# Performance work log

Measured on AMD Instinct MI355X. Metric: run time of the kernel, lower is better.

## Reference

```python
import jax, jax.numpy as jnp
import numpy as np

B, T, H = 2, 2048, 1024
NH_R, HD_R = 4, 256            # RWKV6 heads / head_dim
EXP, HD_M = 2, 64
DI = EXP * H                   # mamba inner = 2048
NH_M = DI // HD_M              # 32 mamba heads
DS = 128                       # mamba d_state
CK = 4                         # causal conv kernel
FFN = 4 * H
EPS = 1e-6


def rms(x, w, eps=EPS):
    return w * x * jax.lax.rsqrt(jnp.mean(x * x, -1, keepdims=True) + eps)


def setup_inputs() -> dict:
    key = jax.random.key(0)
    ks = iter(jax.random.split(key, 32))
    def w(shape, scale=0.02):
        return jax.random.normal(next(ks), shape, jnp.float32) * scale
    return dict(
        x=w((B, T, H), 1.0),
        ln_w=jnp.ones((H,), jnp.float32),
        r_w=w((H, H)), k_w=w((H, H)), v_w=w((H, H)), g_w=w((H, H)), dw_w=w((H, H)),
        u=w((NH_R, HD_R), 0.5),
        gn_w=jnp.ones((H,), jnp.float32),
        o_w=w((H, H)),
        in_proj=w((H, 2 * DI + 2 * DS + NH_M)),
        conv_w=w((DI + 2 * DS, CK), 0.1),
        conv_b=jnp.zeros((DI + 2 * DS,), jnp.float32),
        dt_bias=w((NH_M,), 0.1),
        A_log=jnp.log(jnp.arange(1, NH_M + 1, dtype=jnp.float32)),
        D_m=w((NH_M,), 0.5),
        m_norm_w=jnp.ones((DI,), jnp.float32),
        out_proj=w((DI, H)),
        gate_w=jnp.zeros((2 * H, 1), jnp.float32),   # zero-init per module
        gate_b=jnp.zeros((1,), jnp.float32),         # logit(0.5) = 0
        ffn_ln_w=jnp.ones((H,), jnp.float32),
        ffn_w1=w((H, FFN)),
        ffn_w2=w((FFN, H)),
    )


def _rwkv6(nx, r_w, k_w, v_w, g_w, dw_w, u, gn_w, o_w):
    r = (nx @ r_w).reshape(B, T, NH_R, HD_R)
    k = (nx @ k_w).reshape(B, T, NH_R, HD_R)
    v = (nx @ v_w).reshape(B, T, NH_R, HD_R)
    g = jax.nn.silu(nx @ g_w)                                  # output gate
    wdec = jnp.exp(-jnp.exp(nx @ dw_w)).reshape(B, T, NH_R, HD_R)  # data-dep decay in (0,1)
    tm = lambda a: a.transpose(1, 0, 2, 3)                     # [T,B,h,d]

    def step(S, inp):  # S: [B,h,K,V]
        rt, kt, vt, wt = inp
        kv = kt[..., :, None] * vt[..., None, :]
        o = jnp.einsum('bhk,bhkv->bhv', rt, S + u[..., :, None] * kv)
        return wt[..., :, None] * S + kv, o

    S0 = jnp.zeros((B, NH_R, HD_R, HD_R), nx.dtype)
    _, o = jax.lax.scan(step, S0, (tm(r), tm(k), tm(v), tm(wdec)))
    o = o.transpose(1, 0, 2, 3)                                # [B,T,h,d]
    o = o * jax.lax.rsqrt(jnp.mean(o * o, -1, keepdims=True) + EPS)  # per-head RMS (group norm)
    o = o.reshape(B, T, H) * gn_w
    return (o * g) @ o_w


def _mamba2(nx, in_proj, conv_w, conv_b, dt_bias, A_log, D_m, m_norm_w, out_proj):
    zxbcdt = nx @ in_proj
    z, xBC, dt = jnp.split(zxbcdt, [DI, 2 * DI + 2 * DS], axis=-1)
    xp = jnp.pad(xBC, ((0, 0), (CK - 1, 0), (0, 0)))           # causal depthwise conv
    xBC = sum(xp[:, i:i + T, :] * conv_w[:, i] for i in range(CK)) + conv_b
    xBC = jax.nn.silu(xBC)
    xm, Bm, Cm = jnp.split(xBC, [DI, DI + DS], axis=-1)
    xm = xm.reshape(B, T, NH_M, HD_M)
    dt = jax.nn.softplus(dt + dt_bias)                          # [B,T,nh]
    A = -jnp.exp(A_log)                                         # [nh]

    def step(h, inp):  # h: [B,nh,hd,ds]
        xt, Bt, Ct, dtt = inp
        h = h * jnp.exp(dtt * A)[..., None, None] + (dtt[..., None] * xt)[..., None] * Bt[:, None, None, :]
        y = jnp.einsum('bhds,bs->bhd', h, Ct)
        return h, y

    h0 = jnp.zeros((B, NH_M, HD_M, DS), nx.dtype)
    _, y = jax.lax.scan(step, h0, (xm.transpose(1, 0, 2, 3), Bm.transpose(1, 0, 2), Cm.transpose(1, 0, 2), dt.transpose(1, 0, 2)))
    y = y.transpose(1, 0, 2, 3) + D_m[None, None, :, None] * xm
    y = y.reshape(B, T, DI)
    y = rms(y * jax.nn.silu(z), m_norm_w)                       # gated RMSNorm
    return y @ out_proj


def reference(x, ln_w, r_w, k_w, v_w, g_w, dw_w, u, gn_w, o_w,
              in_proj, conv_w, conv_b, dt_bias, A_log, D_m, m_norm_w, out_proj,
              gate_w, gate_b, ffn_ln_w, ffn_w1, ffn_w2):
    nx = rms(x, ln_w)
    o_r = _rwkv6(nx, r_w, k_w, v_w, g_w, dw_w, u, gn_w, o_w)
    o_m = _mamba2(nx, in_proj, conv_w, conv_b, dt_bias, A_log, D_m, m_norm_w, out_proj)
    gate = jax.nn.sigmoid(jnp.concatenate([o_r, o_m], -1) @ gate_w + gate_b)  # [B,T,1]
    x = x + gate * o_r + (1.0 - gate) * o_m
    x = x + jax.nn.gelu(rms(x, ffn_ln_w) @ ffn_w1, approximate=False) @ ffn_w2
    return x
```

## Files before the change

### kernel.cpp

```cpp
#include <hip/hip_runtime.h>
#include <hip/hip_bf16.h>
#include <stdint.h>

#define B_ 2
#define T_ 2048
#define H_ 1024
#define M_ 4096
#define DI 2048
#define DS 128
#define CONVD 2304
#define LD2 4480
#define EPS_ 1e-6f

typedef __bf16 bf16x8 __attribute__((ext_vector_type(8)));
typedef float f32x4 __attribute__((ext_vector_type(4)));
typedef uint32_t u32x4 __attribute__((ext_vector_type(4)));

__device__ __forceinline__ unsigned short f2bfu(float f) {
    union { float f; uint32_t u; } a; a.f = f;
    uint32_t r = a.u + 0x7FFFu + ((a.u >> 16) & 1u);
    return (unsigned short)(r >> 16);
}
__device__ __forceinline__ float bfu2f(unsigned short u) {
    union { uint32_t u; float f; } a; a.u = ((uint32_t)u) << 16; return a.f;
// ... 288 lines not shown
                bg[n] = *(const bf16x8*)((const char*)Bs + (lin ^ ((col & 7) << 4)));
            }
#pragma unroll
            for (int m = 0; m < 4; m++)
#pragma unroll
                for (int n = 0; n < 4; n++)
                    acc[m][n] = __builtin_amdgcn_mfma_f32_16x16x32_bf16(af[m], bg[n], acc[m][n], 0, 0, 0);
        }
    }
    const int seg = n0 >> 10;
#pragma unroll
    for (int m = 0; m < 4; m++) {
#pragma unroll
        for (int r = 0; r < 4; r++) {
            size_t row = (size_t)(m0 + wm + m * 16 + fg * 4 + r);
#pragma unroll
            for (int n = 0; n < 4; n++) {
                int gcol = n0 + wn + n * 16 + fr;
                float v = acc[m][n][r];
                if (n0 < 5120) {
                    size_t idx = row * 1024 + (gcol & 1023);
                    if (seg == 0) RB[idx] = f2bfu(v);
                    else if (seg == 1) KB[idx] = f2bfu(v);
                    else if (seg == 2) VB[idx] = f2bfu(v);
                    else if (seg == 3) GB[idx] = f2bfu(siluf(v));
                    else WF[idx] = expf(-expf(v));
                } else {
                    C2B[row * 4480 + (gcol - 5120)] = f2bfu(v);
                }
            }
        }
    }
}

__global__ __launch_bounds__(256) void k_rwkv_prep(unsigned short* __restrict__ RB, unsigned short* __restrict__ KB,
                                                   const float* __restrict__ WF, const float* __restrict__ u,
                                                   unsigned short* __restrict__ KDt, unsigned short* __restrict__ QLb,
                                                   float* __restrict__ DDb) {
    __shared__ float red[16][257];
    __shared__ float red2[16][17];
    const int c = blockIdx.x, bh = blockIdx.y;
    const int b = bh >> 2, h = bh & 3;
    const int k = threadIdx.x;
    const size_t m0 = (size_t)b * T_ + c * 16;
    const int hk = h * 256 + k;
    const float uv = u[hk];
    float Q = 1.f;
    float kd[16];
#pragma unroll
    for (int s = 0; s < 16; s++) {
        size_t off = (m0 + s) * H_ + hk;
        float r = bfu2f(RB[off]);
        float kv = bfu2f(KB[off]);
        float w = WF[off];
        RB[off] = f2bfu(r * Q);
        Q = fmaxf(Q * w, 1e-35f);
        float kdv = kv / Q;
        kd[s] = kdv;
        KB[off] = f2bfu(kdv);
        red[s][k] = r * uv * kv;
    }
    QLb[((size_t)(b * 128 + c)) * 1024 + hk] = f2bfu(Q);
    size_t kt0 = (((size_t)(b * 128 + c)) * 1024 + hk) * 16;
#pragma unroll
    for (int s = 0; s < 16; s++) KDt[kt0 + s] = f2bfu(kd[s]);
    __syncthreads();
    {
        int s = threadIdx.x >> 4, part = threadIdx.x & 15;
        float ps = 0.f;
#pragma unroll
        for (int j = 0; j < 16; j++) ps += red[s][part * 16 + j];
        red2[s][part] = ps;
    }
    __syncthreads();
    if (threadIdx.x < 32) {
        int s = threadIdx.x & 15, half = threadIdx.x >> 4;
        float d = 0.f;
#pragma unroll
        for (int j = 0; j < 8; j++) d += red2[s][half * 8 + j];
        DDb[(((size_t)bh * 128 + c) * 2 + half) * 16 + s] = d;
    }
}

__global__ __launch_bounds__(256) void k_rwkv_carry(const unsigned short* __restrict__ KD, const unsigned short* __restrict__ VB,
                                                    const unsigned short* __restrict__ QLb, unsigned short* __restrict__ Scc) {
    __shared__ unsigned short kds[16][256];
    __shared__ float lv[16][4];
    const int vg = blockIdx.x, bh = blockIdx.y;
    const int b = bh >> 2, h = bh & 3;
    const int k = threadIdx.x;
    const int hk = h * 256 + k;
    const size_t baseM = (size_t)b * T_;
    float s0 = 0.f, s1 = 0.f, s2 = 0.f, s3 = 0.f;
    for (int c = 0; c < 128; ++c) {
        size_t m0 = baseM + c * 16;
        if ((c & 7) == 0 && c > 0) {
            int cc = c >> 3;
            size_t sb = ((size_t)(bh * 16 + cc) * 256 + vg * 4) * 256 + k;
            Scc[sb] = f2bfu(s0); Scc[sb + 256] = f2bfu(s1);
            Scc[sb + 512] = f2bfu(s2); Scc[sb + 768] = f2bfu(s3);
        }
        __syncthreads();
#pragma unroll
        for (int it = 0; it < 2; ++it) {
            int i = threadIdx.x + it * 256;
            int row = i >> 5, col8 = (i & 31) * 8;
            *(u32x4*)&kds[row][col8] = *(const u32x4*)(KD + (m0 + row) * H_ + h * 256 + col8);
        }
        if (threadIdx.x < 64) {
            int t = threadIdx.x >> 2, j = threadIdx.x & 3;
            lv[t][j] = bfu2f(VB[(m0 + t) * H_ + h * 256 + vg * 4 + j]);
        }
        __syncthreads();
        float a0 = 0.f, a1 = 0.f, a2 = 0.f, a3 = 0.f;
#pragma unroll
        for (int t = 0; t < 16; t++) {
            float kdv = bfu2f(kds[t][k]);
            a0 = fmaf(kdv, lv[t][0], a0);
            a1 = fmaf(kdv, lv[t][1], a1);
            a2 = fmaf(kdv, lv[t][2], a2);
            a3 = fmaf(kdv, lv[t][3], a3);
        }
        float ql = bfu2f(QLb[((size_t)(b * 128 + c)) * 1024 + hk]);
        s0 = (s0 + a0) * ql; s1 = (s1 + a1) * ql;
        s2 = (s2 + a2) * ql; s3 = (s3 + a3) * ql;
    }
}

__global__ __launch_bounds__(256) void k_rwkv_out(const unsigned short* __restrict__ RT, const unsigned short* __restrict__ KD,
                                                  const unsigned short* __restrict__ KDt, const unsigned short* __restrict__ VB,
                                                  const unsigned short* __restrict__ QLb, const float* __restrict__ DDb,
                                                  const unsigned short* __restrict__ Scc,
                                                  float* __restrict__ P0, float* __restrict__ P1) {
    __shared__ unsigned short Sb[64][136];
    __shared__ unsigned short VT[64][24];
    __shared__ unsigned short Ab[16][24];
    __shared__ float dls[16];
    const int tid = threadIdx.x;
    const int vt = blockIdx.x, cc = blockIdx.y;
    const int bh = blockIdx.z >> 1, kh = blockIdx.z & 1;
    const int b = bh >> 2, h = bh & 3;
    const int wave = tid >> 6, lane = tid & 63;
    const int l16 = lane & 15, lq = lane >> 4;
    const int wv0 = wave * 16;
    const int hk0 = h * 256 + kh * 128;
    const int hv = h * 256 + vt * 64;
    const int aoff = (lq < 2) ? lq * 8 : 0;
    float* __restrict__ OP = kh ? P1 : P0;
    f32x4 sreg[8];
    if (cc == 0) {
#pragma unroll
        for (int kt = 0; kt < 8; kt++) sreg[kt] = (f32x4)(0.f);
        for (int i = tid; i < 64 * 136 / 8; i += 256) ((u32x4*)Sb)[i] = (u32x4)(0u);
    } else {
        size_t sbase = ((size_t)(bh * 16 + cc) * 256 + vt * 64);
        for (int i = tid; i < 1024; i += 256) {
            int v = i >> 4, k8 = (i & 15) * 8;
            *(u32x4*)&Sb[v][k8] = *(const u32x4*)(Scc + (sbase + v) * 256 + kh * 128 + k8);
        }
#pragma unroll
        for (int kt = 0; kt < 8; kt++) {
            ushort4 w4 = *(const ushort4*)(Scc + (sbase + wv0 + l16) * 256 + kh * 128 + kt * 16 + lq * 4);
            sreg[kt][0] = bfu2f(w4.x); sreg[kt][1] = bfu2f(w4.y);
            sreg[kt][2] = bfu2f(w4.z); sreg[kt][3] = bfu2f(w4.w);
        }
    }
    __syncthreads();

    for (int fc = 0; fc < 8; ++fc) {
        const int c = cc * 8 + fc;
        const size_t m0 = (size_t)b * T_ + c * 16;
        const size_t bc = (size_t)(b * 128 + c);
        if (fc > 0) __syncthreads();
        {
            int st = tid >> 4, v4 = (tid & 15) * 4;
            ushort4 v4v = *(const ushort4*)(VB + (m0 + st) * H_ + hv + v4);
            VT[v4 + 0][st] = v4v.x; VT[v4 + 1][st] = v4v.y;
            VT[v4 + 2][st] = v4v.z; VT[v4 + 3][st] = v4v.w;
            if (tid < 16) dls[tid] = DDb[(((size_t)bh * 128 + c) * 2 + kh) * 16 + tid];
        }
        __syncthreads();
        const size_t rowA = (m0 + l16) * H_ + hk0;
        bf16x8 rtf[4];
#pragma unroll
        for (int ks = 0; ks < 4; ks++) rtf[ks] = *(const bf16x8*)(RT + rowA + ks * 32 + lq * 8);
        f32x4 Aacc = (f32x4)(0.f);
#pragma unroll
        for (int ks = 0; ks < 4; ks++) {
            bf16x8 kdf = *(const bf16x8*)(KD + rowA + ks * 32 + lq * 8);
            Aacc = __builtin_amdgcn_mfma_f32_16x16x32_bf16(rtf[ks], kdf, Aacc, 0, 0, 0);
        }
        f32x4 oacc = (f32x4)(0.f);
#pragma unroll
        for (int ks = 0; ks < 4; ks++) {
            bf16x8 sbf = *(const bf16x8*)(&Sb[wv0 + l16][ks * 32 + lq * 8]);
            oacc = __builtin_amdgcn_mfma_f32_16x16x32_bf16(rtf[ks], sbf, oacc, 0, 0, 0);
        }
#pragma unroll
        for (int r = 0; r < 4; r++) {
            int t = lq * 4 + r, s = l16;
            float av = (s < t) ? Aacc[r] : ((s == t) ? dls[t] : 0.f);
            Ab[t][s] = f2bfu(av);
        }
        bf16x8 abf_t = *(const bf16x8*)(&Ab[l16][aoff]);
        bf16x8 vtf_t = *(const bf16x8*)(&VT[wv0 + l16][aoff]);
        bf16x8 abf = (lq < 2) ? abf_t : zero8();
        bf16x8 vtf = (lq < 2) ? vtf_t : zero8();
        oacc = __builtin_amdgcn_mfma_f32_16x16x32_bf16(abf, vtf, oacc, 0, 0, 0);
#pragma unroll
        for (int r = 0; r < 4; r++)
            OP[(m0 + lq * 4 + r) * H_ + hv + wv0 + l16] = oacc[r];
#pragma unroll
        for (int kt = 0; kt < 8; kt++) {
            const unsigned short* kp = KDt + (((bc * 1024) + hk0 + kt * 16 + l16) << 4) + aoff;
            bf16x8 kdtf_t = *(const bf16x8*)kp;
            bf16x8 kdtf = (lq < 2) ? kdtf_t : zero8();
            sreg[kt] = __builtin_amdgcn_mfma_f32_16x16x32_bf16(kdtf, vtf, sreg[kt], 0, 0, 0);
            ushort4 q4 = *(const ushort4*)(QLb + bc * 1024 + hk0 + kt * 16 + lq * 4);
            sreg[kt][0] *= bfu2f(q4.x); sreg[kt][1] *= bfu2f(q4.y);
            sreg[kt][2] *= bfu2f(q4.z); sreg[kt][3] *= bfu2f(q4.w);
            ushort4 pk;
            pk.x = f2bfu(sreg[kt][0]); pk.y = f2bfu(sreg[kt][1]);
            pk.z = f2bfu(sreg[kt][2]); pk.w = f2bfu(sreg[kt][3]);
            *(ushort4*)(&Sb[wv0 + l16][kt * 16 + lq * 4]) = pk;
        }
    }
}

__global__ __launch_bounds__(256) void k_rwkv_post(const float* __restrict__ P0, const float* __restrict__ P1,
                                                   const float* __restrict__ gn_w, unsigned short* __restrict__ g_io) {
    int m = blockIdx.x, tid = threadIdx.x;
    int wave = tid >> 6, lane = tid & 63;
    size_t base = (size_t)m * H_ + wave * 256 + lane * 4;
    int col = wave * 256 + lane * 4;
    float4 a = *(const float4*)(P0 + base);
    float4 b4 = *(const float4*)(P1 + base);
    float4 v; v.x = a.x + b4.x; v.y = a.y + b4.y; v.z = a.z + b4.z; v.w = a.w + b4.w;
    float ss = v.x * v.x + v.y * v.y + v.z * v.z + v.w * v.w;
#pragma unroll
    for (int off = 32; off; off >>= 1) ss += __shfl_xor(ss, off);
    float scale = rsqrtf(ss * (1.f / 256.f) + EPS_);
    float4 gn = *(const float4*)(gn_w + col);
    ushort4 gb4 = *(const ushort4*)(g_io + base);
    ushort4 out;
    out.x = f2bfu(v.x * scale * gn.x * bfu2f(gb4.x));
    out.y = f2bfu(v.y * scale * gn.y * bfu2f(gb4.y));
    out.z = f2bfu(v.z * scale * gn.z * bfu2f(gb4.z));
    out.w = f2bfu(v.w * scale * gn.w * bfu2f(gb4.w));
    *(ushort4*)(g_io + base) = out;
}

__global__ __launch_bounds__(256) void k_conv(const unsigned short* __restrict__ C2B, const float* __restrict__ conv_w,
                                              const float* __restrict__ conv_b, unsigned short* __restrict__ XB,
                                              float* __restrict__ BCF) {
    int m = blockIdx.y;
    int c = blockIdx.x * 256 + threadIdx.x;
    int b = m >> 11, t = m & 2047;
    float acc = conv_b[c];
#pragma unroll
    for (int i = 0; i < 4; i++) {
        int tt = t - 3 + i;
        if (tt >= 0) acc = fmaf(bfu2f(C2B[((size_t)(b * T_ + tt)) * LD2 + DI + c]), conv_w[c * 4 + i], acc);
    }
    float r = siluf(acc);
    if (c < DI) XB[(size_t)m * DI + c] = f2bfu(r);
    else BCF[(size_t)m * 256 + (c - DI)] = r;
}

__global__ __launch_bounds__(256) void k_mprep(const unsigned short* __restrict__ C2B,
                                               const float* __restrict__ dt_bias, const float* __restrict__ A_log,
                                               float* __restrict__ DT, float* __restrict__ CD,
                                               float* __restrict__ WS, float* __restrict__ WSC,
                                               float* __restrict__ QJ, float* __restrict__ QLf,
                                               float* __restrict__ QC) {
    __shared__ float sums[128], offs[128], ce[16];
    const int bh = blockIdx.x;
    const int b = bh >> 5, h = bh & 31;
    const int c = threadIdx.x;
    const float A = -expf(A_log[h]);
    const float dtb = dt_bias[h];
    float dloc[16], cdl[16];
    if (c < 128) {
        float acc = 0.f;
#pragma unroll
        for (int s = 0; s < 16; s++) {
            size_t m = (size_t)b * T_ + c * 16 + s;
            float draw = bfu2f(C2B[m * LD2 + 4352 + h]) + dtb;
            float dt = draw > 20.f ? draw : log1pf(expf(draw));
            acc += dt;
            dloc[s] = dt; cdl[s] = acc;
        }
        sums[c] = acc;
    }
    __syncthreads();
    if (threadIdx.x == 0) {
        float run = 0.f;
        for (int i = 0; i < 128; i++) { offs[i] = run; run += sums[i]; }
    }
    __syncthreads();
    if (threadIdx.x < 16) {
        int last = threadIdx.x * 8 + 7;
        ce[threadIdx.x] = offs[last] + sums[last];
    }
    __syncthreads();
    if (c < 128) {
        float off = offs[c];
        float cd15 = off + cdl[15];
        float ceC = ce[c >> 3];
        QLf[bh * 128 + c] = expf(fminf(A * cdl[15], 0.f));
        size_t base = (size_t)bh * 2048 + c * 16;
#pragma unroll
        for (int s = 0; s < 16; s++) {
            float cdg = off + cdl[s];
            DT[base + s] = dloc[s];
            CD[base + s] = cdg;
            QJ[base + s] = expf(fminf(A * (cdg - off), 0.f));
            WS[base + s] = expf(fminf(A * (cd15 - cdg), 0.f)) * dloc[s];
            WSC[base + s] = expf(fminf(A * (ceC - cdg), 0.f)) * dloc[s];
        }
    }
    if (threadIdx.x < 16) {
        float prev = threadIdx.x ? ce[threadIdx.x - 1] : 0.f;
        QC[bh * 16 + threadIdx.x] = expf(fminf(A * (ce[threadIdx.x] - prev), 0.f));
    }
}

__global__ __launch_bounds__(64) void k_amask(const float* __restrict__ BCF,
                                              const float* __restrict__ CD, const float* __restrict__ DT,
                                              const float* __restrict__ A_log,
                                              unsigned short* __restrict__ AM) {
    const int c = blockIdx.x, bh = blockIdx.y;
    const int b = bh >> 5, h = bh & 31;
    const int lane = threadIdx.x;
    const int l16 = lane & 15, lq = lane >> 4;
    const float A = -expf(A_log[h]);
    const size_t m = (size_t)b * T_ + c * 16 + l16;
    f32x4 Aacc = (f32x4)(0.f);
#pragma unroll
    for (int ks = 0; ks < 4; ks++) {
        bf16x8 cf, bf;
        const float* cr = BCF + m * 256 + 128 + ks * 32 + lq * 8;
        const float* br = BCF + m * 256 + ks * 32 + lq * 8;
#pragma unroll
        for (int i = 0; i < 8; i++) { cf[i] = (__bf16)cr[i]; bf[i] = (__bf16)br[i]; }
        Aacc = __builtin_amdgcn_mfma_f32_16x16x32_bf16(cf, bf, Aacc, 0, 0, 0);
    }
    size_t base = ((size_t)bh * 128 + c) * 256;
    size_t tb = (size_t)bh * 2048 + c * 16;
    float cds = CD[tb + l16];
    float dts = DT[tb + l16];
#pragma unroll
    for (int r = 0; r < 4; r++) {
        int j = lq * 4 + r;
        float av = 0.f;
        if (l16 <= j) {
            float cdj = CD[tb + j];
            av = Aacc[r] * expf(fminf(A * (cdj - cds), 0.f)) * dts;
        }
        AM[base + j * 16 + l16] = f2bfu(av);
    }
}

__global__ __launch_bounds__(256) void k_mcarry(const float* __restrict__ BCF, const unsigned short* __restrict__ XB,
                                                const float* __restrict__ WSC, const float* __restrict__ QC,
                                                unsigned short* __restrict__ MSCC) {
    __shared__ float Bsf[64][128];
    __shared__ unsigned short BWt[128][72];
    __shared__ unsigned short XT[16][72];
    __shared__ float wsl[64];
    const int tid = threadIdx.x;
    const int dq = blockIdx.x, bh = blockIdx.y;
    const int b = bh >> 5, h = bh & 31;
    const int wave = tid >> 6, lane = tid & 63;
    const int l16 = lane & 15, lq = lane >> 4;
    const size_t baseM = (size_t)b * T_;
    f32x4 sreg[2];
    sreg[0] = (f32x4)(0.f); sreg[1] = (f32x4)(0.f);

    for (int cc = 0; cc < 15; ++cc) {
        float qC = QC[bh * 16 + cc];
        sreg[0] *= qC; sreg[1] *= qC;
        for (int sub = 0; sub < 2; ++sub) {
            int t0g = cc * 128 + sub * 64;
            __syncthreads();
            if (tid < 64) wsl[tid] = WSC[(size_t)bh * 2048 + t0g + tid];
#pragma unroll
            for (int i = 0; i < 8; i++) {
                int idx4 = tid + i * 256;
                int t = idx4 >> 5, s4 = (idx4 & 31) * 4;
                *(float4*)&Bsf[t][s4] = *(const float4*)(BCF + (baseM + t0g + t) * 256 + s4);
            }
#pragma unroll
            for (int i = 0; i < 4; i++) {
                int idx = tid + i * 256;
                int t = idx >> 4, d = idx & 15;
                XT[d][t] = XB[(baseM + t0g + t) * DI + h * 64 + dq * 16 + d];
            }
            __syncthreads();
            {
                int sg = tid >> 1;
                int tb = (tid & 1) * 32;
#pragma unroll
                for (int q = 0; q < 8; q++) {
                    int tt = tb + q * 4;
                    ushort4 v;
                    v.x = f2bfu(Bsf[tt + 0][sg] * wsl[tt + 0]);
                    v.y = f2bfu(Bsf[tt + 1][sg] * wsl[tt + 1]);
                    v.z = f2bfu(Bsf[tt + 2][sg] * wsl[tt + 2]);
                    v.w = f2bfu(Bsf[tt + 3][sg] * wsl[tt + 3]);
                    *(ushort4*)&BWt[sg][tt] = v;
                }
            }
            __syncthreads();
#pragma unroll
            for (int st = 0; st < 2; st++) {
#pragma unroll
                for (int ks = 0; ks < 2; ks++) {
                    bf16x8 bwf = *(const bf16x8*)&BWt[wave * 32 + st * 16 + l16][ks * 32 + lq * 8];
                    bf16x8 xtf = *(const bf16x8*)&XT[l16][ks * 32 + lq * 8];
                    sreg[st] = __builtin_amdgcn_mfma_f32_16x16x32_bf16(bwf, xtf, sreg[st], 0, 0, 0);
                }
            }
        }
        size_t dbase = ((size_t)(bh * 16 + cc + 1) * 64 + dq * 16 + l16) * 128;
#pragma unroll
        for (int st = 0; st < 2; st++) {
            ushort4 pk;
            pk.x = f2bfu(sreg[st][0]); pk.y = f2bfu(sreg[st][1]);
            pk.z = f2bfu(sreg[st][2]); pk.w = f2bfu(sreg[st][3]);
            *(ushort4*)(MSCC + dbase + wave * 32 + st * 16 + lq * 4) = pk;
        }
    }
}

__global__ __launch_bounds__(256) void k_mout(const float* __restrict__ BCF, const unsigned short* __restrict__ XB,
                                              const unsigned short* __restrict__ AM,
                                              const float* __restrict__ QJ, const float* __restrict__ WS,
                                              const float* __restrict__ QLf, const unsigned short* __restrict__ MSCC,
                                              unsigned short* __restrict__ Y) {
    __shared__ unsigned short Sb[64][136];
    __shared__ unsigned short Cs[16][136];
    __shared__ unsigned short BWt[128][24];
    __shared__ unsigned short XT[64][24];
    __shared__ unsigned short Ab[16][24];
    __shared__ float qjl[16], wsl[16], qLl;
    const int tid = threadIdx.x;
    const int cc = blockIdx.x, bh = blockIdx.y;
    const int b = bh >> 5, h = bh & 31;
    const int wave = tid >> 6, lane = tid & 63;
    const int l16 = lane & 15, lq = lane >> 4;
    const int wv0 = wave * 16;
    const int aoff = (lq < 2) ? lq * 8 : 0;
    const size_t baseM = (size_t)b * T_;
    f32x4 sreg[8];
    if (cc == 0) {
#pragma unroll
        for (int kt = 0; kt < 8; kt++) sreg[kt] = (f32x4)(0.f);
        for (int i = tid; i < 64 * 136 / 8; i += 256) ((u32x4*)Sb)[i] = (u32x4)(0u);
    } else {
        size_t sbase = (size_t)(bh * 16 + cc) * 64;
        for (int i = tid; i < 1024; i += 256) {
            int d = i >> 4, s8 = (i & 15) * 8;
            *(u32x4*)&Sb[d][s8] = *(const u32x4*)(MSCC + (sbase + d) * 128 + s8);
        }
#pragma unroll
        for (int kt = 0; kt < 8; kt++) {
            ushort4 w4 = *(const ushort4*)(MSCC + (sbase + wv0 + l16) * 128 + kt * 16 + lq * 4);
            sreg[kt][0] = bfu2f(w4.x); sreg[kt][1] = bfu2f(w4.y);
            sreg[kt][2] = bfu2f(w4.z); sreg[kt][3] = bfu2f(w4.w);
        }
    }

    for (int fc = 0; fc < 8; ++fc) {
        const int c = cc * 8 + fc;
        const size_t m0 = baseM + c * 16;
        __syncthreads();
        if (tid < 16) {
            size_t tb = (size_t)bh * 2048 + c * 16 + tid;
            qjl[tid] = QJ[tb];
            wsl[tid] = WS[tb];
            if (tid == 0) qLl = QLf[bh * 128 + c];
        }
        {
            int j = tid >> 4, s = tid & 15;
            Ab[j][s] = AM[((size_t)bh * 128 + c) * 256 + tid];
        }
#pragma unroll
        for (int i = 0; i < 8; i++) {
            int idx = tid + i * 256;
            int t = idx >> 7, sig = idx & 127;
            Cs[t][sig] = f2bfu(BCF[(m0 + t) * 256 + 128 + sig]);
        }
#pragma unroll
        for (int i = 0; i < 4; i++) {
            int idx = tid + i * 256;
            int t = idx >> 6, d = idx & 63;
            XT[d][t] = XB[(m0 + t) * DI + h * 64 + d];
        }
        __syncthreads();
#pragma unroll
        for (int i = 0; i < 8; i++) {
            int idx = tid + i * 256;
            int t = idx >> 7, sig = idx & 127;
            BWt[sig][t] = f2bfu(BCF[(m0 + t) * 256 + sig] * wsl[t]);
        }
        __syncthreads();
        bf16x8 cf[4];
#pragma unroll
        for (int ks = 0; ks < 4; ks++) cf[ks] = *(const bf16x8*)(&Cs[l16][ks * 32 + lq * 8]);
        f32x4 oacc = (f32x4)(0.f);
#pragma unroll
        for (int ks = 0; ks < 4; ks++) {
            bf16x8 sbf = *(const bf16x8*)(&Sb[wv0 + l16][ks * 32 + lq * 8]);
            oacc = __builtin_amdgcn_mfma_f32_16x16x32_bf16(cf[ks], sbf, oacc, 0, 0, 0);
        }
#pragma unroll
        for (int r = 0; r < 4; r++) oacc[r] *= qjl[lq * 4 + r];
        bf16x8 abf_t = *(const bf16x8*)(&Ab[l16][aoff]);
        bf16x8 xtf_t = *(const bf16x8*)(&XT[wv0 + l16][aoff]);
        bf16x8 abf = (lq < 2) ? abf_t : zero8();
        bf16x8 xtf = (lq < 2) ? xtf_t : zero8();
        oacc = __builtin_amdgcn_mfma_f32_16x16x32_bf16(abf, xtf, oacc, 0, 0, 0);
#pragma unroll
        for (int r = 0; r < 4; r++)
            Y[(m0 + lq * 4 + r) * DI + h * 64 + wv0 + l16] = f2bfu(oacc[r]);
        float qL = qLl;
#pragma unroll
        for (int kt = 0; kt < 8; kt++) {
            sreg[kt] *= qL;
            bf16x8 bwf_t = *(const bf16x8*)(&BWt[kt * 16 + l16][aoff]);
            bf16x8 bwf = (lq < 2) ? bwf_t : zero8();
            sreg[kt] = __builtin_amdgcn_mfma_f32_16x16x32_bf16(bwf, xtf, sreg[kt], 0, 0, 0);
            ushort4 pk;
            pk.x = f2bfu(sreg[kt][0]); pk.y = f2bfu(sreg[kt][1]);
            pk.z = f2bfu(sreg[kt][2]); pk.w = f2bfu(sreg[kt][3]);
            *(ushort4*)(&Sb[wv0 + l16][kt * 16 + lq * 4]) = pk;
        }
    }
}

__global__ __launch_bounds__(256) void k_mamba_post(unsigned short* __restrict__ y_io,
                                                    const unsigned short* __restrict__ XB,
                                                    const unsigned short* __restrict__ C2B, const float* __restrict__ D_m,
                                                    const float* __restrict__ mnw) {
    __shared__ float red[4];
    int m = blockIdx.x, tid = threadIdx.x;
    int j0 = tid * 8;
    const float Dv = D_m[j0 >> 6];
    ushort4 ya = *(const ushort4*)(y_io + (size_t)m * DI + j0);
    ushort4 yb = *(const ushort4*)(y_io + (size_t)m * DI + j0 + 4);
    ushort4 xa = *(const ushort4*)(XB + (size_t)m * DI + j0);
    ushort4 xb = *(const ushort4*)(XB + (size_t)m * DI + j0 + 4);
    ushort4 za = *(const ushort4*)(C2B + (size_t)m * LD2 + j0);
    ushort4 zb = *(const ushort4*)(C2B + (size_t)m * LD2 + j0 + 4);
    float yv[8] = {bfu2f(ya.x), bfu2f(ya.y), bfu2f(ya.z), bfu2f(ya.w),
                   bfu2f(yb.x), bfu2f(yb.y), bfu2f(yb.z), bfu2f(yb.w)};
    float xv[8] = {bfu2f(xa.x), bfu2f(xa.y), bfu2f(xa.z), bfu2f(xa.w), bfu2f(xb.x), bfu2f(xb.y), bfu2f(xb.z), bfu2f(xb.w)};
    float zv[8] = {bfu2f(za.x), bfu2f(za.y), bfu2f(za.z), bfu2f(za.w), bfu2f(zb.x), bfu2f(zb.y), bfu2f(zb.z), bfu2f(zb.w)};
    float val[8];
    float ss = 0.f;
#pragma unroll
    for (int i = 0; i < 8; i++) {
        float v = (yv[i] + Dv * xv[i]) * siluf(zv[i]);
        val[i] = v;
        ss += v * v;
    }
#pragma unroll
    for (int off = 32; off; off >>= 1) ss += __shfl_xor(ss, off);
    if ((tid & 63) == 0) red[tid >> 6] = ss;
    __syncthreads();
    float scale = rsqrtf((red[0] + red[1] + red[2] + red[3]) * (1.f / 2048.f) + EPS_);
    ushort4 oa, ob;
    oa.x = f2bfu(val[0] * scale * mnw[j0 + 0]); oa.y = f2bfu(val[1] * scale * mnw[j0 + 1]);
    oa.z = f2bfu(val[2] * scale * mnw[j0 + 2]); oa.w = f2bfu(val[3] * scale * mnw[j0 + 3]);
    ob.x = f2bfu(val[4] * scale * mnw[j0 + 4]); ob.y = f2bfu(val[5] * scale * mnw[j0 + 5]);
    ob.z = f2bfu(val[6] * scale * mnw[j0 + 6]); ob.w = f2bfu(val[7] * scale * mnw[j0 + 7]);
    *(ushort4*)(y_io + (size_t)m * DI + j0) = oa;
    *(ushort4*)(y_io + (size_t)m * DI + j0 + 4) = ob;
}

__global__ __launch_bounds__(256) void k_mix(const float* __restrict__ x, const float* __restrict__ o_r,
                                             const float* __restrict__ o_m, const float* __restrict__ gw,
                                             const float* __restrict__ gb, const float* __restrict__ flnw,
                                             float* __restrict__ x1, unsigned short* __restrict__ nx2) {
    __shared__ float red[4];
    int m = blockIdx.x, tid = threadIdx.x;
    size_t base = (size_t)m * H_ + tid * 4;
    float4 orv = *(const float4*)(o_r + base);
    float4 omv = *(const float4*)(o_m + base);
    float4 xv = *(const float4*)(x + base);
    float4 g1 = *(const float4*)(gw + tid * 4);
    float4 g2 = *(const float4*)(gw + 1024 + tid * 4);
    float ps = orv.x * g1.x + orv.y * g1.y + orv.z * g1.z + orv.w * g1.w
             + omv.x * g2.x + omv.y * g2.y + omv.z * g2.z + omv.w * g2.w;
#pragma unroll
    for (int off = 32; off; off >>= 1) ps += __shfl_xor(ps, off);
    if ((tid & 63) == 0) red[tid >> 6] = ps;
    __syncthreads();
    float g = 1.f / (1.f + expf(-(red[0] + red[1] + red[2] + red[3] + gb[0])));
    float4 xo;
    xo.x = xv.x + g * orv.x + (1.f - g) * omv.x;
    xo.y = xv.y + g * orv.y + (1.f - g) * omv.y;
    xo.z = xv.z + g * orv.z + (1.f - g) * omv.z;
    xo.w = xv.w + g * orv.w + (1.f - g) * omv.w;
    *(float4*)(x1 + base) = xo;
    float ss = xo.x * xo.x + xo.y * xo.y + xo.z * xo.z + xo.w * xo.w;
#pragma unroll
    for (int off = 32; off; off >>= 1) ss += __shfl_xor(ss, off);
    __syncthreads();
    if ((tid & 63) == 0) red[tid >> 6] = ss;
    __syncthreads();
    float scale = rsqrtf((red[0] + red[1] + red[2] + red[3]) * (1.f / 1024.f) + EPS_);
    float4 wv = *(const float4*)(flnw + tid * 4);
    ushort4 o;
    o.x = f2bfu(xo.x * scale * wv.x); o.y = f2bfu(xo.y * scale * wv.y);
    o.z = f2bfu(xo.z * scale * wv.z); o.w = f2bfu(xo.w * scale * wv.w);
    *(ushort4*)(nx2 + base) = o;
}

extern "C" void kernel_launch(void* const* d_in, const int* in_sizes, int n_in,
                              void* d_out, int out_size, void* d_ws, size_t ws_size,
                              hipStream_t stream) {
    const float* x = (const float*)d_in[0];
    const float* ln_w = (const float*)d_in[1];
    const float* r_w = (const float*)d_in[2];
    const float* k_w = (const float*)d_in[3];
    const float* v_w = (const float*)d_in[4];
    const float* g_w = (const float*)d_in[5];
    const float* dw_w = (const float*)d_in[6];
    const float* u = (const float*)d_in[7];
    const float* gn_w = (const float*)d_in[8];
    const float* o_w = (const float*)d_in[9];
    const float* in_proj = (const float*)d_in[10];
    const float* conv_w = (const float*)d_in[11];
    const float* conv_b = (const float*)d_in[12];
    const float* dt_bias = (const float*)d_in[13];
    const float* A_log = (const float*)d_in[14];
    const float* D_m = (const float*)d_in[15];
    const float* m_norm_w = (const float*)d_in[16];
    const float* out_proj = (const float*)d_in[17];
    const float* gate_w = (const float*)d_in[18];
    const float* gate_b = (const float*)d_in[19];
    const float* ffn_ln_w = (const float*)d_in[20];
    const float* ffn_w1 = (const float*)d_in[21];
    const float* ffn_w2 = (const float*)d_in[22];
    (void)in_sizes; (void)n_in;

    const size_t NEEDED = 192675840ull;
    if (ws_size < NEEDED) {
        hipMemsetAsync(d_out, 0, (size_t)out_size * 4, stream);
        return;
    }
    char* ws = (char*)d_ws;
    unsigned short* WT5 = (unsigned short*)(ws + 0);
    unsigned short* INPT = (unsigned short*)(ws + 10485760);
    unsigned short* QLb = (unsigned short*)(ws + 0);
    float* DDb = (float*)(ws + 524288);
    unsigned short* SCC = (unsigned short*)(ws + 1048576);
    unsigned short* MSCC = (unsigned short*)(ws + 1048576);
    unsigned short* F1T = (unsigned short*)(ws + 0);
    unsigned short* F2T = (unsigned short*)(ws + 10485760);
    unsigned short* OWT = (unsigned short*)(ws + 19660800);
    unsigned short* OPT = (unsigned short*)(ws + 21757952);
    unsigned short* NXB = (unsigned short*)(ws + 25952256);
    unsigned short* KDt = NXB;
    unsigned short* RB = (unsigned short*)(ws + 34340864);
    unsigned short* KB = (unsigned short*)(ws + 42729472);
    unsigned short* VB = (unsigned short*)(ws + 51118080);
    unsigned short* GB = (unsigned short*)(ws + 59506688);
    float* WF = (float*)(ws + 67895296);
    char* MTB = ws + 67895296;
    float* DTt = (float*)(MTB + 0);
    float* CDt = (float*)(MTB + 524288);
    float* WSt = (float*)(MTB + 1048576);
    float* WSCt = (float*)(MTB + 1572864);
    float* QJt = (float*)(MTB + 2097152);
    float* QLft = (float*)(MTB + 2621440);
    float* QCt = (float*)(MTB + 2654208);
    unsigned short* AMt = (unsigned short*)(MTB + 2658304);
    float* OM = (float*)(ws + 34340864);
    unsigned short* MIDB = (unsigned short*)(ws + 51118080);
    unsigned short* C2B = (unsigned short*)(ws + 84672512);
    unsigned short* XB = (unsigned short*)(ws + 121372672);
    float* BCF = (float*)(ws + 138149888);
    float* P0 = (float*)(ws + 142344192);
    float* P1 = (float*)(ws + 159121408);
    unsigned short* YB = (unsigned short*)(ws + 175898624);

    dim3 blk(256);
    k_rms1024<<<M_, blk, 0, stream>>>(x, ln_w, NXB);
    k_transpose6<<<dim3(32, 32, 6), blk, 0, stream>>>(r_w, k_w, v_w, g_w, dw_w, o_w, WT5, OWT);
    k_transpose<<<dim3(140, 32), blk, 0, stream>>>(in_proj, INPT, 1024, 4384, 4480);
    k_transpose<<<dim3(32, 64), blk, 0, stream>>>(out_proj, OPT, 2048, 1024, 1024);
    k_gemm_fused<<<dim3(75, 32), blk, 0, stream>>>(NXB, WT5, RB, KB, VB, GB, WF, C2B);
    k_conv<<<dim3(9, M_), blk, 0, stream>>>(C2B, conv_w, conv_b, XB, BCF);
    k_rwkv_prep<<<dim3(128, 8), blk, 0, stream>>>(RB, KB, WF, u, KDt, QLb, DDb);
    k_mprep<<<64, blk, 0, stream>>>(C2B, dt_bias, A_log, DTt, CDt, WSt, WSCt, QJt, QLft, QCt);
    k_amask<<<dim3(128, 64), dim3(64), 0, stream>>>(BCF, CDt, DTt, A_log, AMt);
    k_rwkv_carry<<<dim3(64, 8), blk, 0, stream>>>(KB, VB, QLb, SCC);
    k_rwkv_out<<<dim3(4, 16, 16), blk, 0, stream>>>(RB, KB, KDt, VB, QLb, DDb, SCC, P0, P1);
    k_rwkv_post<<<M_, blk, 0, stream>>>(P0, P1, gn_w, GB);
    k_mcarry<<<dim3(4, 64), blk, 0, stream>>>(BCF, XB, WSCt, QCt, MSCC);
    k_mout<<<dim3(16, 64), blk, 0, stream>>>(BCF, XB, AMt, QJt, WSt, QLft, MSCC, YB);
    k_mamba_post<<<M_, blk, 0, stream>>>(YB, XB, C2B, D_m, m_norm_w);
    k_transpose<<<dim3(128, 32), blk, 0, stream>>>(ffn_w1, F1T, 1024, 4096, 4096);
    k_transpose<<<dim3(32, 128), blk, 0, stream>>>(ffn_w2, F2T, 4096, 1024, 1024);
    k_gemm_pair<<<dim3(8, 32, 2), blk, 0, stream>>>(GB, OWT, P1, 1024, YB, OPT, OM, 2048);
    k_mix<<<M_, blk, 0, stream>>>(x, P1, OM, gate_w, gate_b, ffn_ln_w, P0, NXB);
    k_gemm<4><<<dim3(32, 32), blk, 0, stream>>>(NXB, F1T, MIDB, nullptr, 4096, 4096, 1024);
    k_gemm<5><<<dim3(8, 32), blk, 0, stream>>>(MIDB, F2T, (float*)d_out, P0, 4096, 1024, 4096);
}
```

Baseline: 908.8 us.

## Merge RWKV and Mamba carry kernels and post kernels into combined launches

Combines the independent RWKV carry (512 blocks) and Mamba carry (256 blocks) kernels into one 768-block launch that branches on block index, so the two low-occupancy serial-scan kernels run concurrently on the GPU. It likewise merges the RWKV group-norm post and Mamba gated-RMSNorm post into one 8192-block launch. MSCC is moved to a separate workspace region (the P0 area) so it no longer aliases SCC, and k_mout is reordered to run before k_rwkv_out. The combined carry kernel uses a shared union buffer sized for the larger branch, which may reduce occupancy for the RWKV half.

Measured after the change: 861.9 us. 1.05x faster.

```diff
diff --git a/kernel.cpp b/kernel.cpp
--- a/kernel.cpp
+++ b/kernel.cpp
@@ -394,48 +394,123 @@
     }
 }
 
-__global__ __launch_bounds__(256) void k_rwkv_carry(const unsigned short* __restrict__ KD, const unsigned short* __restrict__ VB,
-                                                    const unsigned short* __restrict__ QLb, unsigned short* __restrict__ Scc) {
-    __shared__ unsigned short kds[16][256];
-    __shared__ float lv[16][4];
-    const int vg = blockIdx.x, bh = blockIdx.y;
-    const int b = bh >> 2, h = bh & 3;
-    const int k = threadIdx.x;
-    const int hk = h * 256 + k;
-    const size_t baseM = (size_t)b * T_;
-    float s0 = 0.f, s1 = 0.f, s2 = 0.f, s3 = 0.f;
-    for (int c = 0; c < 128; ++c) {
-        size_t m0 = baseM + c * 16;
-        if ((c & 7) == 0 && c > 0) {
-            int cc = c >> 3;
-            size_t sb = ((size_t)(bh * 16 + cc) * 256 + vg * 4) * 256 + k;
-            Scc[sb] = f2bfu(s0); Scc[sb + 256] = f2bfu(s1);
-            Scc[sb + 512] = f2bfu(s2); Scc[sb + 768] = f2bfu(s3);
-        }
-        __syncthreads();
-#pragma unroll
-        for (int it = 0; it < 2; ++it) {
-            int i = threadIdx.x + it * 256;
-            int row = i >> 5, col8 = (i & 31) * 8;
-            *(u32x4*)&kds[row][col8] = *(const u32x4*)(KD + (m0 + row) * H_ + h * 256 + col8);
-        }
-        if (threadIdx.x < 64) {
-            int t = threadIdx.x >> 2, j = threadIdx.x & 3;
-            lv[t][j] = bfu2f(VB[(m0 + t) * H_ + h * 256 + vg * 4 + j]);
-        }
-        __syncthreads();
-        float a0 = 0.f, a1 = 0.f, a2 = 0.f, a3 = 0.f;
-#pragma unroll
-        for (int t = 0; t < 16; t++) {
-            float kdv = bfu2f(kds[t][k]);
-            a0 = fmaf(kdv, lv[t][0], a0);
-            a1 = fmaf(kdv, lv[t][1], a1);
-            a2 = fmaf(kdv, lv[t][2], a2);
-            a3 = fmaf(kdv, lv[t][3], a3);
-        }
-        float ql = bfu2f(QLb[((size_t)(b * 128 + c)) * 1024 + hk]);
-        s0 = (s0 + a0) * ql; s1 = (s1 + a1) * ql;
-        s2 = (s2 + a2) * ql; s3 = (s3 + a3) * ql;
+__global__ __launch_bounds__(256) void k_carry2(const unsigned short* __restrict__ KD, const unsigned short* __restrict__ VB,
+                                                const unsigned short* __restrict__ QLb, unsigned short* __restrict__ Scc,
+                                                const float* __restrict__ BCF, const unsigned short* __restrict__ XB,
+                                                const float* __restrict__ WSC, const float* __restrict__ QC,
+                                                unsigned short* __restrict__ MSCC) {
+    __shared__ alignas(16) float smem[13440];
+    const int tid = threadIdx.x;
+    if (blockIdx.x < 512) {
+        unsigned short* kds = (unsigned short*)smem;
+        float* lv = smem + 2048;
+        const int vg = blockIdx.x & 63, bh = blockIdx.x >> 6;
+        const int b = bh >> 2, h = bh & 3;
+        const int k = tid;
+        const int hk = h * 256 + k;
+        const size_t baseM = (size_t)b * T_;
+        float s0 = 0.f, s1 = 0.f, s2 = 0.f, s3 = 0.f;
+        for (int c = 0; c < 128; ++c) {
+            size_t m0 = baseM + c * 16;
+            if ((c & 7) == 0 && c > 0) {
+                int cc = c >> 3;
+                size_t sb = ((size_t)(bh * 16 + cc) * 256 + vg * 4) * 256 + k;
+                Scc[sb] = f2bfu(s0); Scc[sb + 256] = f2bfu(s1);
+                Scc[sb + 512] = f2bfu(s2); Scc[sb + 768] = f2bfu(s3);
+            }
+            __syncthreads();
+#pragma unroll
+            for (int it = 0; it < 2; ++it) {
+                int i = tid + it * 256;
+                int row = i >> 5, col8 = (i & 31) * 8;
+                *(u32x4*)(kds + row * 256 + col8) = *(const u32x4*)(KD + (m0 + row) * H_ + h * 256 + col8);
+            }
+            if (tid < 64) {
+                int t = tid >> 2, j = tid & 3;
+                lv[t * 4 + j] = bfu2f(VB[(m0 + t) * H_ + h * 256 + vg * 4 + j]);
+            }
+            __syncthreads();
+            float a0 = 0.f, a1 = 0.f, a2 = 0.f, a3 = 0.f;
+#pragma unroll
+            for (int t = 0; t < 16; t++) {
+                float kdv = bfu2f(kds[t * 256 + k]);
+                a0 = fmaf(kdv, lv[t * 4 + 0], a0);
+                a1 = fmaf(kdv, lv[t * 4 + 1], a1);
+                a2 = fmaf(kdv, lv[t * 4 + 2], a2);
+                a3 = fmaf(kdv, lv[t * 4 + 3], a3);
+            }
+            float ql = bfu2f(QLb[((size_t)(b * 128 + c)) * 1024 + hk]);
+            s0 = (s0 + a0) * ql; s1 = (s1 + a1) * ql;
+            s2 = (s2 + a2) * ql; s3 = (s3 + a3) * ql;
+        }
+    } else {
+        float* Bsf = smem;
+        unsigned short* BWt = (unsigned short*)((char*)smem + 32768);
+        unsigned short* XT = (unsigned short*)((char*)smem + 51200);
+        float* wsl = (float*)((char*)smem + 53504);
+        int zz = blockIdx.x - 512;
+        const int dq = zz & 3, bh = zz >> 2;
+        const int b = bh >> 5, h = bh & 31;
+        const int wave = tid >> 6, lane = tid & 63;
+        const int l16 = lane & 15, lq = lane >> 4;
+        const size_t baseM = (size_t)b * T_;
+        f32x4 sreg[2];
+        sreg[0] = (f32x4)(0.f); sreg[1] = (f32x4)(0.f);
+
+        for (int cc = 0; cc < 15; ++cc) {
+            float qC = QC[bh * 16 + cc];
+            sreg[0] *= qC; sreg[1] *= qC;
+            for (int sub = 0; sub < 2; ++sub) {
+                int t0g = cc * 128 + sub * 64;
+                __syncthreads();
+                if (tid < 64) wsl[tid] = WSC[(size_t)bh * 2048 + t0g + tid];
+#pragma unroll
+                for (int i = 0; i < 8; i++) {
+                    int idx4 = tid + i * 256;
+                    int t = idx4 >> 5, s4 = (idx4 & 31) * 4;
+                    *(float4*)(Bsf + t * 128 + s4) = *(const float4*)(BCF + (baseM + t0g + t) * 256 + s4);
+                }
+#pragma unroll
+                for (int i = 0; i < 4; i++) {
+                    int idx = tid + i * 256;
+                    int t = idx >> 4, d = idx & 15;
+                    XT[d * 72 + t] = XB[(baseM + t0g + t) * DI + h * 64 + dq * 16 + d];
+                }
+                __syncthreads();
+                {
+                    int sg = tid >> 1;
+                    int tb = (tid & 1) * 32;
+#pragma unroll
+                    for (int q = 0; q < 8; q++) {
+                        int tt = tb + q * 4;
+                        ushort4 v;
+                        v.x = f2bfu(Bsf[(tt + 0) * 128 + sg] * wsl[tt + 0]);
+                        v.y = f2bfu(Bsf[(tt + 1) * 128 + sg] * wsl[tt + 1]);
+                        v.z = f2bfu(Bsf[(tt + 2) * 128 + sg] * wsl[tt + 2]);
+                        v.w = f2bfu(Bsf[(tt + 3) * 128 + sg] * wsl[tt + 3]);
+                        *(ushort4*)(BWt + sg * 72 + tt) = v;
+                    }
+                }
+                __syncthreads();
+#pragma unroll
+                for (int st = 0; st < 2; st++) {
+#pragma unroll
+                    for (int ks = 0; ks < 2; ks++) {
+                        bf16x8 bwf = *(const bf16x8*)(BWt + (wave * 32 + st * 16 + l16) * 72 + ks * 32 + lq * 8);
+                        bf16x8 xtf = *(const bf16x8*)(XT + l16 * 72 + ks * 32 + lq * 8);
+                        sreg[st] = __builtin_amdgcn_mfma_f32_16x16x32_bf16(bwf, xtf, sreg[st], 0, 0, 0);
+                    }
+                }
+            }
+            size_t dbase = ((size_t)(bh * 16 + cc + 1) * 64 + dq * 16 + l16) * 128;
+#pragma unroll
+            for (int st = 0; st < 2; st++) {
+                ushort4 pk;
+                pk.x = f2bfu(sreg[st][0]); pk.y = f2bfu(sreg[st][1]);
+                pk.z = f2bfu(sreg[st][2]); pk.w = f2bfu(sreg[st][3]);
+                *(ushort4*)(MSCC + dbase + wave * 32 + st * 16 + lq * 4) = pk;
+            }
+        }
     }
 }
 
@@ -539,29 +614,6 @@
     }
 }
 
-__global__ __launch_bounds__(256) void k_rwkv_post(const float* __restrict__ P0, const float* __restrict__ P1,
-                                                   const float* __restrict__ gn_w, unsigned short* __restrict__ g_io) {
-    int m = blockIdx.x, tid = threadIdx.x;
-    int wave = tid >> 6, lane = tid & 63;
-    size_t base = (size_t)m * H_ + wave * 256 + lane * 4;
-    int col = wave * 256 + lane * 4;
-    float4 a = *(const float4*)(P0 + base);
-    float4 b4 = *(const float4*)(P1 + base);
-    float4 v; v.x = a.x + b4.x; v.y = a.y + b4.y; v.z = a.z + b4.z; v.w = a.w + b4.w;
-    float ss = v.x * v.x + v.y * v.y + v.z * v.z + v.w * v.w;
-#pragma unroll
-    for (int off = 32; off; off >>= 1) ss += __shfl_xor(ss, off);
-    float scale = rsqrtf(ss * (1.f / 256.f) + EPS_);
-    float4 gn = *(const float4*)(gn_w + col);
-    ushort4 gb4 = *(const ushort4*)(g_io + base);
-    ushort4 out;
-    out.x = f2bfu(v.x * scale * gn.x * bfu2f(gb4.x));
-    out.y = f2bfu(v.y * scale * gn.y * bfu2f(gb4.y));
-    out.z = f2bfu(v.z * scale * gn.z * bfu2f(gb4.z));
-    out.w = f2bfu(v.w * scale * gn.w * bfu2f(gb4.w));
-    *(ushort4*)(g_io + base) = out;
-}
-
 __global__ __launch_bounds__(256) void k_conv(const unsigned short* __restrict__ C2B, const float* __restrict__ conv_w,
                                               const float* __restrict__ conv_b, unsigned short* __restrict__ XB,
                                               float* __restrict__ BCF) {
@@ -670,78 +722,6 @@
             av = Aacc[r] * expf(fminf(A * (cdj - cds), 0.f)) * dts;
         }
         AM[base + j * 16 + l16] = f2bfu(av);
-    }
-}
-
-__global__ __launch_bounds__(256) void k_mcarry(const float* __restrict__ BCF, const unsigned short* __restrict__ XB,
-                                                const float* __restrict__ WSC, const float* __restrict__ QC,
-                                                unsigned short* __restrict__ MSCC) {
-    __shared__ float Bsf[64][128];
-    __shared__ unsigned short BWt[128][72];
-    __shared__ unsigned short XT[16][72];
-    __shared__ float wsl[64];
-    const int tid = threadIdx.x;
-    const int dq = blockIdx.x, bh = blockIdx.y;
-    const int b = bh >> 5, h = bh & 31;
-    const int wave = tid >> 6, lane = tid & 63;
-    const int l16 = lane & 15, lq = lane >> 4;
-    const size_t baseM = (size_t)b * T_;
-    f32x4 sreg[2];
-    sreg[0] = (f32x4)(0.f); sreg[1] = (f32x4)(0.f);
-
-    for (int cc = 0; cc < 15; ++cc) {
-        float qC = QC[bh * 16 + cc];
-        sreg[0] *= qC; sreg[1] *= qC;
-        for (int sub = 0; sub < 2; ++sub) {
-            int t0g = cc * 128 + sub * 64;
-            __syncthreads();
-            if (tid < 64) wsl[tid] = WSC[(size_t)bh * 2048 + t0g + tid];
-#pragma unroll
-            for (int i = 0; i < 8; i++) {
-                int idx4 = tid + i * 256;
-                int t = idx4 >> 5, s4 = (idx4 & 31) * 4;
-                *(float4*)&Bsf[t][s4] = *(const float4*)(BCF + (baseM + t0g + t) * 256 + s4);
-            }
-#pragma unroll
-            for (int i = 0; i < 4; i++) {
-                int idx = tid + i * 256;
-                int t = idx >> 4, d = idx & 15;
-                XT[d][t] = XB[(baseM + t0g + t) * DI + h * 64 + dq * 16 + d];
-            }
-            __syncthreads();
-            {
-                int sg = tid >> 1;
-                int tb = (tid & 1) * 32;
-#pragma unroll
-                for (int q = 0; q < 8; q++) {
-                    int tt = tb + q * 4;
-                    ushort4 v;
-                    v.x = f2bfu(Bsf[tt + 0][sg] * wsl[tt + 0]);
-                    v.y = f2bfu(Bsf[tt + 1][sg] * wsl[tt + 1]);
-                    v.z = f2bfu(Bsf[tt + 2][sg] * wsl[tt + 2]);
-                    v.w = f2bfu(Bsf[tt + 3][sg] * wsl[tt + 3]);
-                    *(ushort4*)&BWt[sg][tt] = v;
-                }
-            }
-            __syncthreads();
-#pragma unroll
-            for (int st = 0; st < 2; st++) {
-#pragma unroll
-                for (int ks = 0; ks < 2; ks++) {
-                    bf16x8 bwf = *(const bf16x8*)&BWt[wave * 32 + st * 16 + l16][ks * 32 + lq * 8];
-                    bf16x8 xtf = *(const bf16x8*)&XT[l16][ks * 32 + lq * 8];
-                    sreg[st] = __builtin_amdgcn_mfma_f32_16x16x32_bf16(bwf, xtf, sreg[st], 0, 0, 0);
-                }
-            }
-        }
-        size_t dbase = ((size_t)(bh * 16 + cc + 1) * 64 + dq * 16 + l16) * 128;
-#pragma unroll
-        for (int st = 0; st < 2; st++) {
-            ushort4 pk;
-            pk.x = f2bfu(sreg[st][0]); pk.y = f2bfu(sreg[st][1]);
-            pk.z = f2bfu(sreg[st][2]); pk.w = f2bfu(sreg[st][3]);
-            *(ushort4*)(MSCC + dbase + wave * 32 + st * 16 + lq * 4) = pk;
-        }
     }
 }
 
@@ -851,44 +831,68 @@
     }
 }
 
-__global__ __launch_bounds__(256) void k_mamba_post(unsigned short* __restrict__ y_io,
-                                                    const unsigned short* __restrict__ XB,
-                                                    const unsigned short* __restrict__ C2B, const float* __restrict__ D_m,
-                                                    const float* __restrict__ mnw) {
+__global__ __launch_bounds__(256) void k_post2(const float* __restrict__ P0, const float* __restrict__ P1,
+                                               const float* __restrict__ gn_w, unsigned short* __restrict__ g_io,
+                                               unsigned short* __restrict__ y_io, const unsigned short* __restrict__ XB,
+                                               const unsigned short* __restrict__ C2B, const float* __restrict__ D_m,
+                                               const float* __restrict__ mnw) {
     __shared__ float red[4];
-    int m = blockIdx.x, tid = threadIdx.x;
-    int j0 = tid * 8;
-    const float Dv = D_m[j0 >> 6];
-    ushort4 ya = *(const ushort4*)(y_io + (size_t)m * DI + j0);
-    ushort4 yb = *(const ushort4*)(y_io + (size_t)m * DI + j0 + 4);
-    ushort4 xa = *(const ushort4*)(XB + (size_t)m * DI + j0);
-    ushort4 xb = *(const ushort4*)(XB + (size_t)m * DI + j0 + 4);
-    ushort4 za = *(const ushort4*)(C2B + (size_t)m * LD2 + j0);
-    ushort4 zb = *(const ushort4*)(C2B + (size_t)m * LD2 + j0 + 4);
-    float yv[8] = {bfu2f(ya.x), bfu2f(ya.y), bfu2f(ya.z), bfu2f(ya.w),
-                   bfu2f(yb.x), bfu2f(yb.y), bfu2f(yb.z), bfu2f(yb.w)};
-    float xv[8] = {bfu2f(xa.x), bfu2f(xa.y), bfu2f(xa.z), bfu2f(xa.w), bfu2f(xb.x), bfu2f(xb.y), bfu2f(xb.z), bfu2f(xb.w)};
-    float zv[8] = {bfu2f(za.x), bfu2f(za.y), bfu2f(za.z), bfu2f(za.w), bfu2f(zb.x), bfu2f(zb.y), bfu2f(zb.z), bfu2f(zb.w)};
-    float val[8];
-    float ss = 0.f;
-#pragma unroll
-    for (int i = 0; i < 8; i++) {
-        float v = (yv[i] + Dv * xv[i]) * siluf(zv[i]);
-        val[i] = v;
-        ss += v * v;
-    }
-#pragma unroll
-    for (int off = 32; off; off >>= 1) ss += __shfl_xor(ss, off);
-    if ((tid & 63) == 0) red[tid >> 6] = ss;
-    __syncthreads();
-    float scale = rsqrtf((red[0] + red[1] + red[2] + red[3]) * (1.f / 2048.f) + EPS_);
-    ushort4 oa, ob;
-    oa.x = f2bfu(val[0] * scale * mnw[j0 + 0]); oa.y = f2bfu(val[1] * scale * mnw[j0 + 1]);
-    oa.z = f2bfu(val[2] * scale * mnw[j0 + 2]); oa.w = f2bfu(val[3] * scale * mnw[j0 + 3]);
-    ob.x = f2bfu(val[4] * scale * mnw[j0 + 4]); ob.y = f2bfu(val[5] * scale * mnw[j0 + 5]);
-    ob.z = f2bfu(val[6] * scale * mnw[j0 + 6]); ob.w = f2bfu(val[7] * scale * mnw[j0 + 7]);
-    *(ushort4*)(y_io + (size_t)m * DI + j0) = oa;
-    *(ushort4*)(y_io + (size_t)m * DI + j0 + 4) = ob;
+    const int tid = threadIdx.x;
+    if (blockIdx.x < 4096) {
+        int m = blockIdx.x;
+        int wave = tid >> 6, lane = tid & 63;
+        size_t base = (size_t)m * H_ + wave * 256 + lane * 4;
+        int col = wave * 256 + lane * 4;
+        float4 a = *(const float4*)(P0 + base);
+        float4 b4 = *(const float4*)(P1 + base);
+        float4 v; v.x = a.x + b4.x; v.y = a.y + b4.y; v.z = a.z + b4.z; v.w = a.w + b4.w;
+        float ss = v.x * v.x + v.y * v.y + v.z * v.z + v.w * v.w;
+#pragma unroll
+        for (int off = 32; off; off >>= 1) ss += __shfl_xor(ss, off);
+        float scale = rsqrtf(ss * (1.f / 256.f) + EPS_);
+        float4 gn = *(const float4*)(gn_w + col);
+        ushort4 gb4 = *(const ushort4*)(g_io + base);
+        ushort4 out;
+        out.x = f2bfu(v.x * scale * gn.x * bfu2f(gb4.x));
+        out.y = f2bfu(v.y * scale * gn.y * bfu2f(gb4.y));
+        out.z = f2bfu(v.z * scale * gn.z * bfu2f(gb4.z));
+        out.w = f2bfu(v.w * scale * gn.w * bfu2f(gb4.w));
+        *(ushort4*)(g_io + base) = out;
+    } else {
+        int m = blockIdx.x - 4096;
+        int j0 = tid * 8;
+        const float Dv = D_m[j0 >> 6];
+        ushort4 ya = *(const ushort4*)(y_io + (size_t)m * DI + j0);
+        ushort4 yb = *(const ushort4*)(y_io + (size_t)m * DI + j0 + 4);
+        ushort4 xa = *(const ushort4*)(XB + (size_t)m * DI + j0);
+        ushort4 xb = *(const ushort4*)(XB + (size_t)m * DI + j0 + 4);
+        ushort4 za = *(const ushort4*)(C2B + (size_t)m * LD2 + j0);
+        ushort4 zb = *(const ushort4*)(C2B + (size_t)m * LD2 + j0 + 4);
+        float yv[8] = {bfu2f(ya.x), bfu2f(ya.y), bfu2f(ya.z), bfu2f(ya.w),
+                       bfu2f(yb.x), bfu2f(yb.y), bfu2f(yb.z), bfu2f(yb.w)};
+        float xv[8] = {bfu2f(xa.x), bfu2f(xa.y), bfu2f(xa.z), bfu2f(xa.w), bfu2f(xb.x), bfu2f(xb.y), bfu2f(xb.z), bfu2f(xb.w)};
+        float zv[8] = {bfu2f(za.x), bfu2f(za.y), bfu2f(za.z), bfu2f(za.w), bfu2f(zb.x), bfu2f(zb.y), bfu2f(zb.z), bfu2f(zb.w)};
+        float val[8];
+        float ss = 0.f;
+#pragma unroll
+        for (int i = 0; i < 8; i++) {
+            float v = (yv[i] + Dv * xv[i]) * siluf(zv[i]);
+            val[i] = v;
+            ss += v * v;
+        }
+#pragma unroll
+        for (int off = 32; off; off >>= 1) ss += __shfl_xor(ss, off);
+        if ((tid & 63) == 0) red[tid >> 6] = ss;
+        __syncthreads();
+        float scale = rsqrtf((red[0] + red[1] + red[2] + red[3]) * (1.f / 2048.f) + EPS_);
+        ushort4 oa, ob;
+        oa.x = f2bfu(val[0] * scale * mnw[j0 + 0]); oa.y = f2bfu(val[1] * scale * mnw[j0 + 1]);
+        oa.z = f2bfu(val[2] * scale * mnw[j0 + 2]); oa.w = f2bfu(val[3] * scale * mnw[j0 + 3]);
+        ob.x = f2bfu(val[4] * scale * mnw[j0 + 4]); ob.y = f2bfu(val[5] * scale * mnw[j0 + 5]);
+        ob.z = f2bfu(val[6] * scale * mnw[j0 + 6]); ob.w = f2bfu(val[7] * scale * mnw[j0 + 7]);
+        *(ushort4*)(y_io + (size_t)m * DI + j0) = oa;
+        *(ushort4*)(y_io + (size_t)m * DI + j0 + 4) = ob;
+    }
 }
 
 __global__ __launch_bounds__(256) void k_mix(const float* __restrict__ x, const float* __restrict__ o_r,
@@ -969,7 +973,6 @@
     unsigned short* QLb = (unsigned short*)(ws + 0);
     float* DDb = (float*)(ws + 524288);
     unsigned short* SCC = (unsigned short*)(ws + 1048576);
-    unsigned short* MSCC = (unsigned short*)(ws + 1048576);
     unsigned short* F1T = (unsigned short*)(ws + 0);
     unsigned short* F2T = (unsigned short*)(ws + 10485760);
     unsigned short* OWT = (unsigned short*)(ws + 19660800);
@@ -997,6 +1000,7 @@
     float* BCF = (float*)(ws + 138149888);
     float* P0 = (float*)(ws + 142344192);
     float* P1 = (float*)(ws + 159121408);
+    unsigned short* MSCC = (unsigned short*)(ws + 142344192);
     unsigned short* YB = (unsigned short*)(ws + 175898624);
 
     dim3 blk(256);
@@ -1009,12 +1013,10 @@
     k_rwkv_prep<<<dim3(128, 8), blk, 0, stream>>>(RB, KB, WF, u, KDt, QLb, DDb);
     k_mprep<<<64, blk, 0, stream>>>(C2B, dt_bias, A_log, DTt, CDt, WSt, WSCt, QJt, QLft, QCt);
     k_amask<<<dim3(128, 64), dim3(64), 0, stream>>>(BCF, CDt, DTt, A_log, AMt);
-    k_rwkv_carry<<<dim3(64, 8), blk, 0, stream>>>(KB, VB, QLb, SCC);
+    k_carry2<<<768, blk, 0, stream>>>(KB, VB, QLb, SCC, BCF, XB, WSCt, QCt, MSCC);
+    k_mout<<<dim3(16, 64), blk, 0, stream>>>(BCF, XB, AMt, QJt, WSt, QLft, MSCC, YB);
     k_rwkv_out<<<dim3(4, 16, 16), blk, 0, stream>>>(RB, KB, KDt, VB, QLb, DDb, SCC, P0, P1);
-    k_rwkv_post<<<M_, blk, 0, stream>>>(P0, P1, gn_w, GB);
-    k_mcarry<<<dim3(4, 64), blk, 0, stream>>>(BCF, XB, WSCt, QCt, MSCC);
-    k_mout<<<dim3(16, 64), blk, 0, stream>>>(BCF, XB, AMt, QJt, WSt, QLft, MSCC, YB);
-    k_mamba_post<<<M_, blk, 0, stream>>>(YB, XB, C2B, D_m, m_norm_w);
+    k_post2<<<8192, blk, 0, stream>>>(P0, P1, gn_w, GB, YB, XB, C2B, D_m, m_norm_w);
     k_transpose<<<dim3(128, 32), blk, 0, stream>>>(ffn_w1, F1T, 1024, 4096, 4096);
     k_transpose<<<dim3(32, 128), blk, 0, stream>>>(ffn_w2, F2T, 4096, 1024, 1024);
     k_gemm_pair<<<dim3(8, 32, 2), blk, 0, stream>>>(GB, OWT, P1, 1024, YB, OPT, OM, 2048);
```
